# Kernel tuning notes

Hardware: AMD Instinct MI355X
Metric: run time of the kernel (lower is better)

The kernel has to match this reference:

```python
import jax, jax.numpy as jnp
import numpy as np

# ode_solve: h_max = 0.125, t in [0, 1] -> n_steps = ceil(1/0.125) = 8 (static)
N_STEPS = 8


def setup_inputs() -> dict:
    key = jax.random.key(0)
    k0, k1, k2 = jax.random.split(key, 3)
    B, D, H = 1024, 256, 1024  # n_batch, dim_z, hidden width of dynamics MLP
    s1 = 1.0 / np.sqrt(D)
    s2 = 1.0 / np.sqrt(H)
    return {
        "z0": jax.random.normal(k0, (B, D), dtype=jnp.float32),
        "t": jnp.array([0.0, 1.0], dtype=jnp.float32),
        "W1": jax.random.normal(k1, (D, H), dtype=jnp.float32) * s1,
        "b1": jnp.zeros((H,), dtype=jnp.float32),
        "W2": jax.random.normal(k2, (H, D), dtype=jnp.float32) * s2,
        "b2": jnp.zeros((D,), dtype=jnp.float32),
    }


def reference(z0, t, W1, b1, W2, b2):
    # Dynamics f(z, t): 2-layer tanh MLP (autonomous in t, matching a typical
    # Function_for_ode instantiation).
    def f(z, ti):
        return jnp.tanh(z @ W1 + b1) @ W2 + b2

    h = (t[1] - t[0]) / N_STEPS  # scalar step size

    def rk4_step(carry, _):
        z, ti = carry
        k1 = f(z, ti)
        k2 = f(z + k1 * (h / 2), ti + h / 2)
        k3 = f(z + k2 * (h / 2), ti + h / 2)
        k4 = f(z + k3 * h, ti + h)
        z_new = z + (k1 + 2 * k2 + 2 * k3 + k4) * (h / 6)
        return (z_new, ti + h), None

    (zT, _), _ = jax.lax.scan(rk4_step, (z0, t[0]), None, length=N_STEPS)
    # NeuralODE.forward with return_whole_sequence=False returns z[-1]
    return zT
```

## Files before the change

### kernel.cpp

```cpp
#include <hip/hip_runtime.h>

typedef _Float16 f16x8 __attribute__((ext_vector_type(8)));
typedef float f32x4 __attribute__((ext_vector_type(4)));

#define Dd 256
#define Hh 1024

__global__ void pack_w1_kernel(const float* __restrict__ W1, _Float16* __restrict__ W1P) {
    int gid = blockIdx.x * 256 + threadIdx.x;
    int h = gid & 1023, d = gid >> 10;
    int w = h >> 7, nt = (h >> 4) & 7, ln = h & 15;
    int kk = d >> 5, q = (d >> 3) & 3, j = d & 7;
    W1P[(((w * 8 + nt) * 8 + kk) * 64 + q * 16 + ln) * 8 + j] = (_Float16)W1[d * 1024 + h];
}
__global__ void pack_w2_kernel(const float* __restrict__ W2, _Float16* __restrict__ W2P) {
    int gid = blockIdx.x * 256 + threadIdx.x;
    int dcol = gid & 255, h = gid >> 8;
    int w = dcol >> 5, t = (dcol >> 4) & 1, ln = dcol & 15;
    int kk = h >> 5, q = (h >> 3) & 3, j = h & 7;
    W2P[(((w * 32 + kk) * 2 + t) * 64 + q * 16 + ln) * 8 + j] = (_Float16)W2[h * 256 + dcol];
}

__global__ __launch_bounds__(512, 2) void ode_kernel(
    const float* __restrict__ z0, const float* __restrict__ tv,
    const float* __restrict__ b1, const float* __restrict__ b2,
    const _Float16* __restrict__ W1P, const _Float16* __restrict__ W2P,
    float* __restrict__ out) {
    __shared__ _Float16 act_lds[16][1032];
    __shared__ _Float16 z_lds[16][264];

    const int tid  = threadIdx.x;
    const int w    = tid >> 6;
    const int lane = tid & 63;
    const int ln   = lane & 15;
    const int q    = lane >> 4;
    const int m0   = blockIdx.x * 16;

    const float h = (tv[1] - tv[0]) * 0.125f;

    float bb1[8];
#pragma unroll
    for (int nt = 0; nt < 8; ++nt) bb1[nt] = b1[w * 128 + nt * 16 + ln];
    float bb2v[2];
#pragma unroll
    for (int t = 0; t < 2; ++t) bb2v[t] = b2[w * 32 + t * 16 + ln];

    const _Float16* W1w = W1P + (size_t)(w * 64) * 512;
    const _Float16* W2w = W2P + (size_t)(w * 64) * 512;

    f16x8 wb[4][4];

#define ISSUE(cc) { const int cm = (cc) & 31;                                        \
    const _Float16* gsrc = (cm < 16) ? (W1w + cm * 2048) : (W2w + (cm - 16) * 2048); \
    _Pragma("unroll")                                                                \
    for (int ii = 0; ii < 4; ++ii)                                                   \
        wb[(cc) & 3][ii] = *(const f16x8*)(gsrc + ii * 512 + lane * 8);              \
    __builtin_amdgcn_sched_barrier(0); }

#define BARRIER() asm volatile("s_waitcnt lgkmcnt(0)\n\ts_barrier" ::: "memory")

    f32x4 z[2], zsum[2];
#pragma unroll
    for (int t = 0; t < 2; ++t)
#pragma unroll
        for (int r = 0; r < 4; ++r)
            z[t][r] = z0[(m0 + q * 4 + r) * Dd + w * 32 + t * 16 + ln];
#pragma unroll
    for (int t = 0; t < 2; ++t)
#pragma unroll
        for (int r = 0; r < 4; ++r)
            z_lds[q * 4 + r][w * 32 + t * 16 + ln] = (_Float16)z[t][r];
    __syncthreads();

    ISSUE(0); ISSUE(1); ISSUE(2); ISSUE(3);

#pragma unroll 1
    for (int ev = 0; ev < 32; ++ev) {
        const int e = ev & 3;

        f16x8 a1[8];
#pragma unroll
        for (int kk = 0; kk < 8; ++kk)
            a1[kk] = *(const f16x8*)&z_lds[ln][kk * 32 + q * 8];

#pragma unroll
        for (int nt = 0; nt < 8; ++nt) {
            f32x4 acc = {0.f, 0.f, 0.f, 0.f};
#pragma unroll
            for (int half = 0; half < 2; ++half) {
                const int c = nt * 2 + half;
#pragma unroll
                for (int i = 0; i < 4; ++i)
                    acc = __builtin_amdgcn_mfma_f32_16x16x32_f16(
                        a1[half * 4 + i], wb[c & 3][i], acc, 0, 0, 0);
                ISSUE(c + 4);
            }
#pragma unroll
            for (int r = 0; r < 4; ++r) {
                float x = acc[r] + bb1[nt];
                float ex = __expf(2.0f * x);
                act_lds[q * 4 + r][w * 128 + nt * 16 + ln] =
                    (_Float16)(1.0f - 2.0f / (ex + 1.0f));
            }
        }
        BARRIER();

        f32x4 acc2[2] = {{0.f, 0.f, 0.f, 0.f}, {0.f, 0.f, 0.f, 0.f}};
#pragma unroll
        for (int cp = 0; cp < 16; ++cp) {
            const int c = 16 + cp;
#pragma unroll
            for (int half = 0; half < 2; ++half) {
                const int kk = cp * 2 + half;
                f16x8 a2 = *(const f16x8*)&act_lds[ln][kk * 32 + q * 8];
#pragma unroll
                for (int t = 0; t < 2; ++t)
                    acc2[t] = __builtin_amdgcn_mfma_f32_16x16x32_f16(
                        a2, wb[c & 3][half * 2 + t], acc2[t], 0, 0, 0);
            }
            ISSUE(c + 4);
        }

#pragma unroll
        for (int t = 0; t < 2; ++t) {
            f32x4 kv, za;
#pragma unroll
            for (int r = 0; r < 4; ++r) kv[r] = acc2[t][r] + bb2v[t];
            if (e == 0) {
                zsum[t] = kv;
            } else if (e == 3) {
#pragma unroll
                for (int r = 0; r < 4; ++r) zsum[t][r] += kv[r];
            } else {
#pragma unroll
                for (int r = 0; r < 4; ++r) zsum[t][r] += 2.0f * kv[r];
            }
            if (e < 3) {
                const float c = (e == 2) ? h : 0.5f * h;
#pragma unroll
                for (int r = 0; r < 4; ++r) za[r] = z[t][r] + c * kv[r];
            } else {
#pragma unroll
                for (int r = 0; r < 4; ++r) {
                    z[t][r] += (h * (1.0f / 6.0f)) * zsum[t][r];
                    za[r] = z[t][r];
                }
            }
#pragma unroll
            for (int r = 0; r < 4; ++r)
                z_lds[q * 4 + r][w * 32 + t * 16 + ln] = (_Float16)za[r];
        }
        BARRIER();
    }

#pragma unroll
    for (int t = 0; t < 2; ++t)
#pragma unroll
        for (int r = 0; r < 4; ++r)
            out[(m0 + q * 4 + r) * Dd + w * 32 + t * 16 + ln] = z[t][r];
#undef ISSUE
#undef BARRIER
}

extern "C" void kernel_launch(void* const* d_in, const int* in_sizes, int n_in,
                              void* d_out, int out_size, void* d_ws, size_t ws_size,
                              hipStream_t stream) {
    const float* z0 = (const float*)d_in[0];
    const float* tv = (const float*)d_in[1];
    const float* W1 = (const float*)d_in[2];
    const float* b1 = (const float*)d_in[3];
    const float* W2 = (const float*)d_in[4];
    const float* b2 = (const float*)d_in[5];
    float* out = (float*)d_out;

    _Float16* W1P = (_Float16*)d_ws;
    _Float16* W2P = W1P + Hh * Dd;

    pack_w1_kernel<<<1024, 256, 0, stream>>>(W1, W1P);
    pack_w2_kernel<<<1024, 256, 0, stream>>>(W2, W2P);

    ode_kernel<<<64, 512, 0, stream>>>(z0, tv, b1, b2, W1P, W2P, out);
}
```

Measured before the change: 525.4 us.

## Double waves per block to 16, halving per-wave N-slice of both GEMMs

Each 16-row block now runs 1024 threads (16 waves) instead of 512, so each wave owns 64 hidden columns and 16 output columns rather than 128 and 32. The weight packing is reordered to match, and the first GEMM loop is restructured to loop over K with four independent accumulators, giving more MFMA independence per step. This halves the serial MFMA chain per wave inside the latency-bound ODE loop. The cost is more waves sharing barriers and each wave streaming weights with less reuse of every A fragment.

```diff
diff --git a/kernel.cpp b/kernel.cpp
--- a/kernel.cpp
+++ b/kernel.cpp
@@ -9,19 +9,19 @@
 __global__ void pack_w1_kernel(const float* __restrict__ W1, _Float16* __restrict__ W1P) {
     int gid = blockIdx.x * 256 + threadIdx.x;
     int h = gid & 1023, d = gid >> 10;
-    int w = h >> 7, nt = (h >> 4) & 7, ln = h & 15;
+    int w = h >> 6, nt = (h >> 4) & 3, ln = h & 15;
     int kk = d >> 5, q = (d >> 3) & 3, j = d & 7;
-    W1P[(((w * 8 + nt) * 8 + kk) * 64 + q * 16 + ln) * 8 + j] = (_Float16)W1[d * 1024 + h];
+    W1P[(((w * 8 + kk) * 4 + nt) * 64 + q * 16 + ln) * 8 + j] = (_Float16)W1[d * 1024 + h];
 }
 __global__ void pack_w2_kernel(const float* __restrict__ W2, _Float16* __restrict__ W2P) {
     int gid = blockIdx.x * 256 + threadIdx.x;
     int dcol = gid & 255, h = gid >> 8;
-    int w = dcol >> 5, t = (dcol >> 4) & 1, ln = dcol & 15;
+    int w = dcol >> 4, ln = dcol & 15;
     int kk = h >> 5, q = (h >> 3) & 3, j = h & 7;
-    W2P[(((w * 32 + kk) * 2 + t) * 64 + q * 16 + ln) * 8 + j] = (_Float16)W2[h * 256 + dcol];
+    W2P[((w * 32 + kk) * 64 + q * 16 + ln) * 8 + j] = (_Float16)W2[h * 256 + dcol];
 }
 
-__global__ __launch_bounds__(512, 2) void ode_kernel(
+__global__ __launch_bounds__(1024) void ode_kernel(
     const float* __restrict__ z0, const float* __restrict__ tv,
     const float* __restrict__ b1, const float* __restrict__ b2,
     const _Float16* __restrict__ W1P, const _Float16* __restrict__ W2P,
@@ -38,38 +38,32 @@
 
     const float h = (tv[1] - tv[0]) * 0.125f;
 
-    float bb1[8];
+    float bb1[4];
 #pragma unroll
-    for (int nt = 0; nt < 8; ++nt) bb1[nt] = b1[w * 128 + nt * 16 + ln];
-    float bb2v[2];
-#pragma unroll
-    for (int t = 0; t < 2; ++t) bb2v[t] = b2[w * 32 + t * 16 + ln];
+    for (int nt = 0; nt < 4; ++nt) bb1[nt] = b1[w * 64 + nt * 16 + ln];
+    const float bb2 = b2[w * 16 + ln];
 
-    const _Float16* W1w = W1P + (size_t)(w * 64) * 512;
-    const _Float16* W2w = W2P + (size_t)(w * 64) * 512;
+    const _Float16* W1w = W1P + (size_t)w * 16384;
+    const _Float16* W2w = W2P + (size_t)w * 16384;
 
     f16x8 wb[4][4];
 
-#define ISSUE(cc) { const int cm = (cc) & 31;                                        \
-    const _Float16* gsrc = (cm < 16) ? (W1w + cm * 2048) : (W2w + (cm - 16) * 2048); \
+#define ISSUE(gg) { const int cm = (gg) & 15;                                        \
+    const _Float16* gsrc = (cm < 8) ? (W1w + cm * 2048) : (W2w + (cm - 8) * 2048);   \
     _Pragma("unroll")                                                                \
     for (int ii = 0; ii < 4; ++ii)                                                   \
-        wb[(cc) & 3][ii] = *(const f16x8*)(gsrc + ii * 512 + lane * 8);              \
+        wb[(gg) & 3][ii] = *(const f16x8*)(gsrc + ii * 512 + lane * 8);              \
     __builtin_amdgcn_sched_barrier(0); }
 
 #define BARRIER() asm volatile("s_waitcnt lgkmcnt(0)\n\ts_barrier" ::: "memory")
 
-    f32x4 z[2], zsum[2];
+    f32x4 z, zsum;
 #pragma unroll
-    for (int t = 0; t < 2; ++t)
+    for (int r = 0; r < 4; ++r)
+        z[r] = z0[(m0 + q * 4 + r) * Dd + w * 16 + ln];
 #pragma unroll
-        for (int r = 0; r < 4; ++r)
-            z[t][r] = z0[(m0 + q * 4 + r) * Dd + w * 32 + t * 16 + ln];
-#pragma unroll
-    for (int t = 0; t < 2; ++t)
-#pragma unroll
-        for (int r = 0; r < 4; ++r)
-            z_lds[q * 4 + r][w * 32 + t * 16 + ln] = (_Float16)z[t][r];
+    for (int r = 0; r < 4; ++r)
+        z_lds[q * 4 + r][w * 16 + ln] = (_Float16)z[r];
     __syncthreads();
 
     ISSUE(0); ISSUE(1); ISSUE(2); ISSUE(3);
@@ -78,86 +72,73 @@
     for (int ev = 0; ev < 32; ++ev) {
         const int e = ev & 3;
 
-        f16x8 a1[8];
+        f32x4 acc[4] = {{0.f,0.f,0.f,0.f},{0.f,0.f,0.f,0.f},
+                        {0.f,0.f,0.f,0.f},{0.f,0.f,0.f,0.f}};
 #pragma unroll
-        for (int kk = 0; kk < 8; ++kk)
-            a1[kk] = *(const f16x8*)&z_lds[ln][kk * 32 + q * 8];
-
+        for (int g = 0; g < 8; ++g) {
+            f16x8 a1 = *(const f16x8*)&z_lds[ln][g * 32 + q * 8];
 #pragma unroll
-        for (int nt = 0; nt < 8; ++nt) {
-            f32x4 acc = {0.f, 0.f, 0.f, 0.f};
+            for (int nt = 0; nt < 4; ++nt)
+                acc[nt] = __builtin_amdgcn_mfma_f32_16x16x32_f16(
+                    a1, wb[g & 3][nt], acc[nt], 0, 0, 0);
+            ISSUE(g + 4);
+        }
 #pragma unroll
-            for (int half = 0; half < 2; ++half) {
-                const int c = nt * 2 + half;
-#pragma unroll
-                for (int i = 0; i < 4; ++i)
-                    acc = __builtin_amdgcn_mfma_f32_16x16x32_f16(
-                        a1[half * 4 + i], wb[c & 3][i], acc, 0, 0, 0);
-                ISSUE(c + 4);
-            }
+        for (int nt = 0; nt < 4; ++nt)
 #pragma unroll
             for (int r = 0; r < 4; ++r) {
-                float x = acc[r] + bb1[nt];
+                float x = acc[nt][r] + bb1[nt];
                 float ex = __expf(2.0f * x);
-                act_lds[q * 4 + r][w * 128 + nt * 16 + ln] =
+                act_lds[q * 4 + r][w * 64 + nt * 16 + ln] =
                     (_Float16)(1.0f - 2.0f / (ex + 1.0f));
             }
-        }
         BARRIER();
 
-        f32x4 acc2[2] = {{0.f, 0.f, 0.f, 0.f}, {0.f, 0.f, 0.f, 0.f}};
+        f32x4 acc2 = {0.f, 0.f, 0.f, 0.f};
 #pragma unroll
-        for (int cp = 0; cp < 16; ++cp) {
-            const int c = 16 + cp;
+        for (int g = 8; g < 16; ++g) {
 #pragma unroll
-            for (int half = 0; half < 2; ++half) {
-                const int kk = cp * 2 + half;
+            for (int i = 0; i < 4; ++i) {
+                const int kk = (g - 8) * 4 + i;
                 f16x8 a2 = *(const f16x8*)&act_lds[ln][kk * 32 + q * 8];
-#pragma unroll
-                for (int t = 0; t < 2; ++t)
-                    acc2[t] = __builtin_amdgcn_mfma_f32_16x16x32_f16(
-                        a2, wb[c & 3][half * 2 + t], acc2[t], 0, 0, 0);
+                acc2 = __builtin_amdgcn_mfma_f32_16x16x32_f16(
+                    a2, wb[g & 3][i], acc2, 0, 0, 0);
             }
-            ISSUE(c + 4);
+            ISSUE(g + 4);
         }
 
+        f32x4 kv, za;
 #pragma unroll
-        for (int t = 0; t < 2; ++t) {
-            f32x4 kv, za;
+        for (int r = 0; r < 4; ++r) kv[r] = acc2[r] + bb2;
+        if (e == 0) {
+            zsum = kv;
+        } else if (e == 3) {
 #pragma unroll
-            for (int r = 0; r < 4; ++r) kv[r] = acc2[t][r] + bb2v[t];
-            if (e == 0) {
-                zsum[t] = kv;
-            } else if (e == 3) {
+            for (int r = 0; r < 4; ++r) zsum[r] += kv[r];
+        } else {
 #pragma unroll
-                for (int r = 0; r < 4; ++r) zsum[t][r] += kv[r];
-            } else {
+            for (int r = 0; r < 4; ++r) zsum[r] += 2.0f * kv[r];
+        }
+        if (e < 3) {
+            const float c = (e == 2) ? h : 0.5f * h;
 #pragma unroll
-                for (int r = 0; r < 4; ++r) zsum[t][r] += 2.0f * kv[r];
+            for (int r = 0; r < 4; ++r) za[r] = z[r] + c * kv[r];
+        } else {
+#pragma unroll
+            for (int r = 0; r < 4; ++r) {
+                z[r] += (h * (1.0f / 6.0f)) * zsum[r];
+                za[r] = z[r];
             }
-            if (e < 3) {
-                const float c = (e == 2) ? h : 0.5f * h;
+        }
 #pragma unroll
-                for (int r = 0; r < 4; ++r) za[r] = z[t][r] + c * kv[r];
-            } else {
-#pragma unroll
-                for (int r = 0; r < 4; ++r) {
-                    z[t][r] += (h * (1.0f / 6.0f)) * zsum[t][r];
-                    za[r] = z[t][r];
-                }
-            }
-#pragma unroll
-            for (int r = 0; r < 4; ++r)
-                z_lds[q * 4 + r][w * 32 + t * 16 + ln] = (_Float16)za[r];
-        }
+        for (int r = 0; r < 4; ++r)
+            z_lds[q * 4 + r][w * 16 + ln] = (_Float16)za[r];
         BARRIER();
     }
 
 #pragma unroll
-    for (int t = 0; t < 2; ++t)
-#pragma unroll
-        for (int r = 0; r < 4; ++r)
-            out[(m0 + q * 4 + r) * Dd + w * 32 + t * 16 + ln] = z[t][r];
+    for (int r = 0; r < 4; ++r)
+        out[(m0 + q * 4 + r) * Dd + w * 16 + ln] = z[r];
 #undef ISSUE
 #undef BARRIER
 }
@@ -179,5 +160,5 @@
     pack_w1_kernel<<<1024, 256, 0, stream>>>(W1, W1P);
     pack_w2_kernel<<<1024, 256, 0, stream>>>(W2, W2P);
 
-    ode_kernel<<<64, 512, 0, stream>>>(z0, tv, b1, b2, W1P, W2P, out);
+    ode_kernel<<<64, 1024, 0, stream>>>(z0, tv, b1, b2, W1P, W2P, out);
 }
```

Result: slower. 679.3 us (+29.3%).
